# Kernel tuning notes

Hardware: AMD Instinct MI355X
Metric: run time of the kernel (lower is better)

Reference implementation:

```python
import jax, jax.numpy as jnp
import numpy as np

EMB = 300      # node embedding dim (GNNGraph default)
NL = 5         # num GNN layers
G = 4096       # number of graphs in batch
ATOM_F, ATOM_V = 9, 128   # OGB-style atom encoder: 9 categorical feats
BOND_F, BOND_V = 3, 8     # OGB-style bond encoder: 3 categorical feats
BN_EPS = 1e-5


def _bn(x, g, b, m, v):
    # BatchNorm1d in eval mode (running stats)
    return (x - m) * jax.lax.rsqrt(v + BN_EPS) * g + b


def _gnn(x, edge_index, edge_attr, batch,
         atom_emb, bond_emb, vn_emb,
         gin_eps, gin_W1, gin_b1, gin_bn1_g, gin_bn1_b, gin_bn1_m, gin_bn1_v,
         gin_W2, gin_b2, bn_g, bn_b, bn_m, bn_v,
         vn_W1, vn_b1, vn_bn1_g, vn_bn1_b, vn_bn1_m, vn_bn1_v,
         vn_W2, vn_b2, vn_bn2_g, vn_bn2_b, vn_bn2_m, vn_bn2_v):
    N = x.shape[0]
    # AtomEncoder / BondEncoder: sum of per-feature embedding lookups
    h = atom_emb[jnp.arange(ATOM_F)[None, :], x].sum(axis=1)          # [N, EMB]
    e = bond_emb[jnp.arange(BOND_F)[None, :], edge_attr].sum(axis=1)  # [E, EMB]
    row, col = edge_index[0], edge_index[1]
    # virtual node embedding, one per graph
    vn = jnp.broadcast_to(vn_emb[0], (G, EMB))
    for l in range(NL):
        h = h + vn[batch]                                   # broadcast virtual node
        # GINConv: message = relu(x_j + edge_emb), aggr = scatter-add at target
        msg = jax.nn.relu(h[row] + e)                       # [E, EMB]
        agg = jax.ops.segment_sum(msg, col, num_segments=N) # [N, EMB]
        t = (1.0 + gin_eps[l]) * h + agg
        t = jnp.dot(t, gin_W1[l]) + gin_b1[l]               # [N, 2*EMB]
        t = jax.nn.relu(_bn(t, gin_bn1_g[l], gin_bn1_b[l], gin_bn1_m[l], gin_bn1_v[l]))
        t = jnp.dot(t, gin_W2[l]) + gin_b2[l]               # [N, EMB]
        hn = _bn(t, bn_g[l], bn_b[l], bn_m[l], bn_v[l])     # outer BatchNorm
        if l < NL - 1:
            hn = jax.nn.relu(hn)                            # (dropout inactive in eval)
            # virtual node update: global_add_pool(h_list[layer]) + vn -> MLP
            pooled = jax.ops.segment_sum(h, batch, num_segments=G) + vn
            u = jnp.dot(pooled, vn_W1[l]) + vn_b1[l]
            u = jax.nn.relu(_bn(u, vn_bn1_g[l], vn_bn1_b[l], vn_bn1_m[l], vn_bn1_v[l]))
            u = jnp.dot(u, vn_W2[l]) + vn_b2[l]
            vn = jax.nn.relu(_bn(u, vn_bn2_g[l], vn_bn2_b[l], vn_bn2_m[l], vn_bn2_v[l]))
        h = hn
    # global_mean_pool over graphs
    counts = jax.ops.segment_sum(jnp.ones((N,), h.dtype), batch, num_segments=G)
    return jax.ops.segment_sum(h, batch, num_segments=G) / jnp.maximum(counts, 1.0)[:, None]


def setup_inputs() -> dict:
    key = jax.random.key(0)
    ks = iter(jax.random.split(key, 64))
    N, E = 100000, 250000
    d = {}
    d['x'] = jax.random.randint(next(ks), (N, ATOM_F), 0, ATOM_V, dtype=jnp.int32)
    d['edge_index'] = jax.random.randint(next(ks), (2, E), 0, N, dtype=jnp.int32)
    d['edge_attr'] = jax.random.randint(next(ks), (E, BOND_F), 0, BOND_V, dtype=jnp.int32)
    d['batch'] = jnp.sort(jax.random.randint(next(ks), (N,), 0, G, dtype=jnp.int32))
    s = 0.05
    d['atom_emb'] = jax.random.normal(next(ks), (ATOM_F, ATOM_V, EMB), jnp.float32) * s
    d['bond_emb'] = jax.random.normal(next(ks), (BOND_F, BOND_V, EMB), jnp.float32) * s
    d['vn_emb'] = jax.random.normal(next(ks), (1, EMB), jnp.float32) * s
    d['gin_eps'] = jax.random.normal(next(ks), (NL,), jnp.float32) * 0.01
    d['gin_W1'] = jax.random.normal(next(ks), (NL, EMB, 2 * EMB), jnp.float32) * s
    d['gin_b1'] = jax.random.normal(next(ks), (NL, 2 * EMB), jnp.float32) * s
    d['gin_bn1_g'] = 1.0 + jax.random.normal(next(ks), (NL, 2 * EMB), jnp.float32) * s
    d['gin_bn1_b'] = jax.random.normal(next(ks), (NL, 2 * EMB), jnp.float32) * s
    d['gin_bn1_m'] = jax.random.normal(next(ks), (NL, 2 * EMB), jnp.float32) * s
    d['gin_bn1_v'] = jax.random.uniform(next(ks), (NL, 2 * EMB), jnp.float32) + 0.5
    d['gin_W2'] = jax.random.normal(next(ks), (NL, 2 * EMB, EMB), jnp.float32) * s
    d['gin_b2'] = jax.random.normal(next(ks), (NL, EMB), jnp.float32) * s
    d['bn_g'] = 1.0 + jax.random.normal(next(ks), (NL, EMB), jnp.float32) * s
    d['bn_b'] = jax.random.normal(next(ks), (NL, EMB), jnp.float32) * s
    d['bn_m'] = jax.random.normal(next(ks), (NL, EMB), jnp.float32) * s
    d['bn_v'] = jax.random.uniform(next(ks), (NL, EMB), jnp.float32) + 0.5
    V = NL - 1
    d['vn_W1'] = jax.random.normal(next(ks), (V, EMB, 2 * EMB), jnp.float32) * s
    d['vn_b1'] = jax.random.normal(next(ks), (V, 2 * EMB), jnp.float32) * s
    d['vn_bn1_g'] = 1.0 + jax.random.normal(next(ks), (V, 2 * EMB), jnp.float32) * s
    d['vn_bn1_b'] = jax.random.normal(next(ks), (V, 2 * EMB), jnp.float32) * s
    d['vn_bn1_m'] = jax.random.normal(next(ks), (V, 2 * EMB), jnp.float32) * s
    d['vn_bn1_v'] = jax.random.uniform(next(ks), (V, 2 * EMB), jnp.float32) + 0.5
    d['vn_W2'] = jax.random.normal(next(ks), (V, 2 * EMB, EMB), jnp.float32) * s
    d['vn_b2'] = jax.random.normal(next(ks), (V, EMB), jnp.float32) * s
    d['vn_bn2_g'] = 1.0 + jax.random.normal(next(ks), (V, EMB), jnp.float32) * s
    d['vn_bn2_b'] = jax.random.normal(next(ks), (V, EMB), jnp.float32) * s
    d['vn_bn2_m'] = jax.random.normal(next(ks), (V, EMB), jnp.float32) * s
    d['vn_bn2_v'] = jax.random.uniform(next(ks), (V, EMB), jnp.float32) + 0.5
    return d


def reference(x, edge_index, edge_attr, batch,
              atom_emb, bond_emb, vn_emb,
              gin_eps, gin_W1, gin_b1, gin_bn1_g, gin_bn1_b, gin_bn1_m, gin_bn1_v,
              gin_W2, gin_b2, bn_g, bn_b, bn_m, bn_v,
              vn_W1, vn_b1, vn_bn1_g, vn_bn1_b, vn_bn1_m, vn_bn1_v,
              vn_W2, vn_b2, vn_bn2_g, vn_bn2_b, vn_bn2_m, vn_bn2_v):
    return _gnn(x, edge_index, edge_attr, batch,
                atom_emb, bond_emb, vn_emb,
                gin_eps, gin_W1, gin_b1, gin_bn1_g, gin_bn1_b, gin_bn1_m, gin_bn1_v,
                gin_W2, gin_b2, bn_g, bn_b, bn_m, bn_v,
                vn_W1, vn_b1, vn_bn1_g, vn_bn1_b, vn_bn1_m, vn_bn1_v,
                vn_W2, vn_b2, vn_bn2_g, vn_bn2_b, vn_bn2_m, vn_bn2_v)
```

## Files before the change

kernel.cpp:

```cpp
#include <hip/hip_runtime.h>
#include <hip/hip_bf16.h>

#define EMBD 300
#define GG   4096
#define NLAY 5
#define KP1  320
#define KP2  640
#define KT2  608
#define NP1  640
#define NP2  384
#define WPER (NP1*KP1 + NP2*KP2)

typedef unsigned short ushort_t;
typedef short short8 __attribute__((ext_vector_type(8)));
typedef short short4v __attribute__((ext_vector_type(4)));
typedef float f32x4 __attribute__((ext_vector_type(4)));

static inline int cdiv(int a, int b) { return (a + b - 1) / b; }


__device__ inline void dma16(const ushort_t* g, ushort_t* l) {
    __builtin_amdgcn_global_load_lds(
        (const __attribute__((address_space(1))) unsigned int*)g,
        (__attribute__((address_space(3))) unsigned int*)l, 16, 0, 0);
}

__device__ inline ushort_t bf16_of(float v) {
    union { __hip_bfloat16 b; ushort_t u; } c;
    c.b = __float2bfloat16(v);
    return c.u;
}

__device__ inline float bf2f(ushort_t u) {
    union { unsigned int i; float f; } c;
    c.i = ((unsigned int)u) << 16;
    return c.f;
}


__global__ void atom_encode_bf(const int* __restrict__ x, const float* __restrict__ aemb,
                               ushort_t* __restrict__ h, int N) {
    int i = blockIdx.x * blockDim.x + threadIdx.x;
    int total = N * 75;
    if (i >= total) return;
    int n = i / 75, d4 = i - n * 75;
    const int* xr = x + n * 9;
    float4 s = make_float4(0.f, 0.f, 0.f, 0.f);
    const float4* a4 = (const float4*)aemb;
#pragma unroll
    for (int f = 0; f < 9; ++f) {
        float4 v = a4[(size_t)((f << 7) + xr[f]) * 75 + d4];
        s.x += v.x; s.y += v.y; s.z += v.z; s.w += v.w;
    }
    short4v o;
    o[0] = (short)bf16_of(s.x); o[1] = (short)bf16_of(s.y);
    o[2] = (short)bf16_of(s.z); o[3] = (short)bf16_of(s.w);
    *(short4v*)(h + (size_t)n * KP1 + d4 * 4) = o;
}

__global__ void init_vn4(const float* __restrict__ vn_emb, float* __restrict__ vn) {
    int i = blockIdx.x * blockDim.x + threadIdx.x;
    if (i >= GG * 75) return;
    ((float4*)vn)[i] = ((const float4*)vn_emb)[i % 75];
}

__global__ void find_starts(const int* __restrict__ batch, int* __restrict__ starts, int N) {
    int g = blockIdx.x * blockDim.x + threadIdx.x;
    if (g > GG) return;
    int lo = 0, hi = N;
    while (lo < hi) {
        int mid = (lo + hi) >> 1;
        if (batch[mid] < g) lo = mid + 1; else hi = mid;
    }
    starts[g] = lo;
}

__global__ void bond_combo(const float* __restrict__ bemb, float* __restrict__ ebsum) {
    int i = blockIdx.x * blockDim.x + threadIdx.x;
    if (i >= 512 * EMBD) return;
    int c = i / EMBD, d = i - c * EMBD;
    int a0 = c >> 6, a1 = (c >> 3) & 7, a2 = c & 7;
    ebsum[i] = bemb[a0 * EMBD + d] + bemb[(8 + a1) * EMBD + d] + bemb[(16 + a2) * EMBD + d];
}

__global__ void conv_all(const float* __restrict__ gW1, const float* __restrict__ gW2,
                         const float* __restrict__ vW1, const float* __restrict__ vW2,
                         ushort_t* __restrict__ wh) {
    int i = blockIdx.x * blockDim.x + threadIdx.x;
    int total = WPER * 9;
    if (i >= total) return;
    int mlp = i / WPER, r = i - mlp * WPER;
    const float *W1, *W2;
    if (mlp < NLAY) {
        W1 = gW1 + (size_t)mlp * EMBD * 2 * EMBD;
        W2 = gW2 + (size_t)mlp * 2 * EMBD * EMBD;
    } else {
        int l = mlp - NLAY;
        W1 = vW1 + (size_t)l * EMBD * 2 * EMBD;
        W2 = vW2 + (size_t)l * 2 * EMBD * EMBD;
    }
    float v;
    if (r < NP1 * KP1) {
        int n = r / KP1, k = r - n * KP1;
        v = (n < 2 * EMBD && k < EMBD) ? W1[(size_t)k * (2 * EMBD) + n] : 0.f;
    } else {
        int r2 = r - NP1 * KP1;
        int n = r2 / KP2, k = r2 - n * KP2;
        v = (n < EMBD && k < 2 * EMBD) ? W2[(size_t)k * EMBD + n] : 0.f;
    }
    wh[i] = bf16_of(v);
}


__global__ void ecount(const int* __restrict__ ei, int* __restrict__ cnt, int E) {
    int e = blockIdx.x * blockDim.x + threadIdx.x;
    if (e >= E) return;
    atomicAdd(&cnt[ei[E + e]], 1);
}

__global__ void scan_part(const int* __restrict__ cnt, int* __restrict__ bsum, int N) {
    __shared__ int sh[256];
    int b = blockIdx.x, t = threadIdx.x;
    int base = b * 1024;
    int s = 0;
    for (int j = t; j < 1024; j += 256) {
        int idx = base + j;
        if (idx < N) s += cnt[idx];
    }
    sh[t] = s;
    __syncthreads();
    for (int d = 128; d > 0; d >>= 1) {
        if (t < d) sh[t] += sh[t + d];
        __syncthreads();
    }
    if (t == 0) bsum[b] = sh[0];
}

__global__ void scan_top(int* __restrict__ bsum, int nb) {
    __shared__ int sh[1024];
    int t = threadIdx.x;
    int v = (t < nb) ? bsum[t] : 0;
    sh[t] = v;
    __syncthreads();
    for (int d = 1; d < 1024; d <<= 1) {
        int u = (t >= d) ? sh[t - d] : 0;
        __syncthreads();
        sh[t] += u;
        __syncthreads();
    }
    if (t < nb) bsum[t] = sh[t] - v;
}

__global__ void scan_final(int* __restrict__ cnt, const int* __restrict__ bsum,
                           int* __restrict__ estart, int* __restrict__ cursor, int N, int E) {
    __shared__ int sh[256];
    int b = blockIdx.x, t = threadIdx.x;
    int base = b * 1024 + t * 4;
    int c[4];
    int s = 0;
#pragma unroll
    for (int j = 0; j < 4; ++j) {
        int idx = base + j;
        c[j] = (idx < N) ? cnt[idx] : 0;
        s += c[j];
    }
    sh[t] = s;
    __syncthreads();
    for (int d = 1; d < 256; d <<= 1) {
        int u = (t >= d) ? sh[t - d] : 0;
        __syncthreads();
        sh[t] += u;
        __syncthreads();
    }
    int run = sh[t] - s + bsum[b];
#pragma unroll
    for (int j = 0; j < 4; ++j) {
        int idx = base + j;
        if (idx < N) { estart[idx] = run; cursor[idx] = run; run += c[j]; }
    }
    if (b == 0 && t == 0) estart[N] = E;
}

__global__ void escatter(const int* __restrict__ ei, const int* __restrict__ ea,
                         int* __restrict__ cursor, int* __restrict__ epack, int E) {
    int e = blockIdx.x * blockDim.x + threadIdx.x;
    if (e >= E) return;
    int c = ei[E + e];
    int p = atomicAdd(&cursor[c], 1);
    epack[p] = (ei[e] << 9) | (ea[3 * e] << 6) | (ea[3 * e + 1] << 3) | ea[3 * e + 2];
}


__global__ void pool_prep(ushort_t* __restrict__ h, const float* __restrict__ vn,
                          const int* __restrict__ starts, ushort_t* __restrict__ vnaB) {
    int g = blockIdx.x * 4 + threadIdx.x / 80;
    int slot = threadIdx.x % 80;
    if (g >= GG || slot >= 75) return;
    float4 vng = ((const float4*)vn)[(size_t)g * 75 + slot];
    int s0 = starts[g], s1 = starts[g + 1];
    float4 s = make_float4(0.f, 0.f, 0.f, 0.f);
    for (int n = s0; n < s1; ++n) {
        short4v* hp = (short4v*)(h + (size_t)n * KP1 + slot * 4);
        short4v hv = *hp;
        float v0 = bf2f((ushort_t)hv[0]) + vng.x;
        float v1 = bf2f((ushort_t)hv[1]) + vng.y;
        float v2 = bf2f((ushort_t)hv[2]) + vng.z;
        float v3 = bf2f((ushort_t)hv[3]) + vng.w;
        short4v o;
        o[0] = (short)bf16_of(v0); o[1] = (short)bf16_of(v1);
        o[2] = (short)bf16_of(v2); o[3] = (short)bf16_of(v3);
        *hp = o;
        s.x += v0; s.y += v1; s.z += v2; s.w += v3;
    }
    short4v o;
    o[0] = (short)bf16_of(s.x + vng.x); o[1] = (short)bf16_of(s.y + vng.y);
    o[2] = (short)bf16_of(s.z + vng.z); o[3] = (short)bf16_of(s.w + vng.w);
    *(short4v*)(vnaB + (size_t)g * KP1 + slot * 4) = o;
}

__global__ void prep_vn(ushort_t* __restrict__ h, const float* __restrict__ vn,
                        const int* __restrict__ batch, int N) {
    int i = blockIdx.x * blockDim.x + threadIdx.x;
    int total = N * 75;
    if (i >= total) return;
    int n = i / 75, d4 = i - n * 75;
    float4 vv = ((const float4*)vn)[(size_t)batch[n] * 75 + d4];
    short4v hv = *(short4v*)(h + (size_t)n * KP1 + d4 * 4);
    short4v o;
    o[0] = (short)bf16_of(bf2f((ushort_t)hv[0]) + vv.x);
    o[1] = (short)bf16_of(bf2f((ushort_t)hv[1]) + vv.y);
    o[2] = (short)bf16_of(bf2f((ushort_t)hv[2]) + vv.z);
    o[3] = (short)bf16_of(bf2f((ushort_t)hv[3]) + vv.w);
    *(short4v*)(h + (size_t)n * KP1 + d4 * 4) = o;
}

__global__ void pool_mean(const ushort_t* __restrict__ h, const int* __restrict__ starts,
                          float* __restrict__ out) {
    int g = blockIdx.x * 4 + threadIdx.x / 80;
    int slot = threadIdx.x % 80;
    if (g >= GG || slot >= 75) return;
    int s0 = starts[g], s1 = starts[g + 1];
    float4 s = make_float4(0.f, 0.f, 0.f, 0.f);
    for (int n = s0; n < s1; ++n) {
        short4v hv = *(const short4v*)(h + (size_t)n * KP1 + slot * 4);
        s.x += bf2f((ushort_t)hv[0]);
        s.y += bf2f((ushort_t)hv[1]);
        s.z += bf2f((ushort_t)hv[2]);
        s.w += bf2f((ushort_t)hv[3]);
    }
    float inv = 1.0f / fmaxf((float)(s1 - s0), 1.0f);
    float4 o = make_float4(s.x * inv, s.y * inv, s.z * inv, s.w * inv);
    ((float4*)out)[(size_t)g * 75 + slot] = o;
}

#define NPB 4

__global__ void aggregate(const ushort_t* __restrict__ h, const float* __restrict__ ebsum,
                          const int* __restrict__ estart, const int* __restrict__ epack,
                          const float* __restrict__ epsp,
                          ushort_t* __restrict__ aggB, int N) {
    int n = blockIdx.x * NPB + threadIdx.x / 80;
    int slot = threadIdx.x % 80;
    if (n >= N) return;
    float4 acc = make_float4(0.f, 0.f, 0.f, 0.f);
    if (slot < 75) {
        const float4* b4 = (const float4*)ebsum;
        float ce = 1.0f + *epsp;
        short4v hv = *(const short4v*)(h + (size_t)n * KP1 + slot * 4);
        acc.x = ce * bf2f((ushort_t)hv[0]);
        acc.y = ce * bf2f((ushort_t)hv[1]);
        acc.z = ce * bf2f((ushort_t)hv[2]);
        acc.w = ce * bf2f((ushort_t)hv[3]);
        int p0 = estart[n], p1 = estart[n + 1];
        int p = p0;
        for (; p + 2 <= p1; p += 2) {
            int e0 = epack[p], e1 = epack[p + 1];
            short4v xv0 = *(const short4v*)(h + (size_t)(e0 >> 9) * KP1 + slot * 4);
            short4v xv1 = *(const short4v*)(h + (size_t)(e1 >> 9) * KP1 + slot * 4);
            float4 ev0 = b4[(size_t)(e0 & 511) * 75 + slot];
            float4 ev1 = b4[(size_t)(e1 & 511) * 75 + slot];
            acc.x += fmaxf(bf2f((ushort_t)xv0[0]) + ev0.x, 0.f) + fmaxf(bf2f((ushort_t)xv1[0]) + ev1.x, 0.f);
            acc.y += fmaxf(bf2f((ushort_t)xv0[1]) + ev0.y, 0.f) + fmaxf(bf2f((ushort_t)xv1[1]) + ev1.y, 0.f);
            acc.z += fmaxf(bf2f((ushort_t)xv0[2]) + ev0.z, 0.f) + fmaxf(bf2f((ushort_t)xv1[2]) + ev1.z, 0.f);
            acc.w += fmaxf(bf2f((ushort_t)xv0[3]) + ev0.w, 0.f) + fmaxf(bf2f((ushort_t)xv1[3]) + ev1.w, 0.f);
        }
        if (p < p1) {
            int e0 = epack[p];
            short4v xv0 = *(const short4v*)(h + (size_t)(e0 >> 9) * KP1 + slot * 4);
            float4 ev0 = b4[(size_t)(e0 & 511) * 75 + slot];
            acc.x += fmaxf(bf2f((ushort_t)xv0[0]) + ev0.x, 0.f);
            acc.y += fmaxf(bf2f((ushort_t)xv0[1]) + ev0.y, 0.f);
            acc.z += fmaxf(bf2f((ushort_t)xv0[2]) + ev0.z, 0.f);
            acc.w += fmaxf(bf2f((ushort_t)xv0[3]) + ev0.w, 0.f);
        }
    }
    short4v bv4;
    bv4[0] = (short)bf16_of(acc.x);
    bv4[1] = (short)bf16_of(acc.y);
    bv4[2] = (short)bf16_of(acc.z);
    bv4[3] = (short)bf16_of(acc.w);
    *(short4v*)(aggB + (size_t)n * KP1 + slot * 4) = bv4;
}

#define BMg 128
#define BNg 128
#define STG (BMg * 32)

__global__ __launch_bounds__(256) void gemm_as(
    const ushort_t* __restrict__ A, int KPA,
    const ushort_t* __restrict__ B, int KPB,
    const float* __restrict__ bias, const float* __restrict__ gg,
    const float* __restrict__ bb, const float* __restrict__ bm,
    const float* __restrict__ bv,
    int Mc, int NnReal, int relu, int nb, int mb,
    float* __restrict__ outF, int ldF,
    ushort_t* __restrict__ outB, int ldP)
{
    __shared__ ushort_t smem[4 * STG];

    int id = blockIdx.x;
    int hi = id / (8 * nb);
    int rem = id - hi * 8 * nb;
    int xcd = rem & 7;
    int nblk = rem >> 3;
    int mblk = hi * 8 + xcd;
    if (mblk >= mb) return;

    const int tid = threadIdx.x;
    const int lane = tid & 63;
    const int w = tid >> 6;
    const int m0 = mblk * BMg;
    const int n0 = nblk * BNg;
    const int wm = (w & 1) * 64;
    const int wn = (w >> 1) * 64;

    const ushort_t* gA[2];
    const ushort_t* gB[2];
    int lbase[2];
#pragma unroll
    for (int i = 0; i < 2; ++i) {
        int s = tid + 256 * i;
        int m = s >> 2, qp = s & 3;
        int q = (qp - (m >> 1)) & 3;
        int msrc = (m0 + m < Mc) ? (m0 + m) : (Mc - 1);
        gA[i] = A + (size_t)msrc * KPA + 8 * q;
        gB[i] = B + (size_t)(n0 + m) * KPB + 8 * q;
        lbase[i] = (w * 64 + 256 * i) * 8;
    }

    f32x4 acc[4][4];
#pragma unroll
    for (int a = 0; a < 4; ++a)
#pragma unroll
        for (int b = 0; b < 4; ++b) acc[a][b] = (f32x4)(0.f);

    const int q = lane >> 4;
    const int c16 = lane & 15;
    const int kt = KPA >> 5;

#pragma unroll
    for (int i = 0; i < 2; ++i) {
        dma16(gA[i], smem + lbase[i]);           gA[i] += 32;
        dma16(gB[i], smem + 2 * STG + lbase[i]); gB[i] += 32;
    }
    __syncthreads();

    for (int t = 0; t < kt; ++t) {
        int cur = t & 1, nxt = cur ^ 1;
        if (t + 1 < kt) {
#pragma unroll
            for (int i = 0; i < 2; ++i) {
                dma16(gA[i], smem + nxt * STG + lbase[i]);       gA[i] += 32;
                dma16(gB[i], smem + (2 + nxt) * STG + lbase[i]); gB[i] += 32;
            }
        }
        const ushort_t* sAc = smem + cur * STG;
        const ushort_t* sBc = smem + (2 + cur) * STG;
        short8 av[4], bhv[4];
#pragma unroll
        for (int tt = 0; tt < 4; ++tt) {
            int m = wm + tt * 16 + c16;
            int q2 = (q + (m >> 1)) & 3;
            av[tt] = *(const short8*)(sAc + m * 32 + q2 * 8);
        }
#pragma unroll
        for (int uu = 0; uu < 4; ++uu) {
            int n = wn + uu * 16 + c16;
            int q2 = (q + (n >> 1)) & 3;
            bhv[uu] = *(const short8*)(sBc + n * 32 + q2 * 8);
        }
#pragma unroll
        for (int tt = 0; tt < 4; ++tt)
#pragma unroll
            for (int uu = 0; uu < 4; ++uu)
                acc[tt][uu] = __builtin_amdgcn_mfma_f32_16x16x32_bf16(av[tt], bhv[uu], acc[tt][uu], 0, 0, 0);
        __syncthreads();
    }

    float sc[4], sh[4];
#pragma unroll
    for (int uu = 0; uu < 4; ++uu) {
        int gn = n0 + wn + uu * 16 + c16;
        if (gn < NnReal) {
            float s = gg[gn] * rsqrtf(bv[gn] + 1e-5f);
            sc[uu] = s;
            sh[uu] = bb[gn] + (bias[gn] - bm[gn]) * sc[uu];
        } else { sc[uu] = 0.f; sh[uu] = 0.f; }
    }

    if (outB) {
        const int rot = q * 16;
#pragma unroll
        for (int uu = 0; uu < 4; ++uu) {
#pragma unroll
            for (int tt = 0; tt < 4; ++tt) {
                int row = wm + tt * 16 + q * 4;
#pragma unroll
                for (int r = 0; r < 4; ++r) {
                    float y = acc[tt][uu][r] * sc[uu] + sh[uu];
                    if (relu) y = fmaxf(y, 0.f);
                    int col_s = (wn + uu * 16 + c16 + rot) & 127;
                    smem[(row + r) * 128 + col_s] = bf16_of(y);
                }
            }
        }
        __syncthreads();
#pragma unroll
        for (int j = 0; j < 8; ++j) {
            int row = j * 16 + q * 4 + w;
            int gm = m0 + row;
            int gcl = c16 * 8;
            if (gm < Mc && n0 + gcl + 8 <= ldP) {
                short8 v = *(const short8*)(smem + row * 128 + ((gcl + rot) & 127));
                *(short8*)(outB + (size_t)gm * ldP + n0 + gcl) = v;
            }
        }
    } else {
#pragma unroll
        for (int uu = 0; uu < 4; ++uu) {
            int gn = n0 + wn + uu * 16 + c16;
#pragma unroll
            for (int tt = 0; tt < 4; ++tt) {
                int rbase = m0 + wm + tt * 16 + q * 4;
#pragma unroll
                for (int r = 0; r < 4; ++r) {
                    int gm = rbase + r;
                    if (gm >= Mc) continue;
                    float y = acc[tt][uu][r] * sc[uu] + sh[uu];
                    if (relu) y = fmaxf(y, 0.f);
                    if (gn < NnReal) outF[(size_t)gm * ldF + gn] = y;
                }
            }
        }
    }
}


struct MlpP {
    const float *b1, *g1, *be1, *m1, *v1;
    const float *b2, *g2, *be2, *m2, *v2;
};

static void run_mlp(hipStream_t stream, const ushort_t* inB, int M,
                    const ushort_t* wh, int mlp,
                    ushort_t* tB, int CH,
                    const MlpP& W, ushort_t* outB, int relu2) {
    const ushort_t* w1 = wh + (size_t)mlp * WPER;
    const ushort_t* w2 = w1 + NP1 * KP1;
    for (int c0 = 0; c0 < M; c0 += CH) {
        int Mc = (M - c0 < CH) ? (M - c0) : CH;
        int mb = cdiv(Mc, BMg);
        int mbp = cdiv(mb, 8) * 8;
        {
            int nb = NP1 / BNg;
            gemm_as<<<nb * mbp, 256, 0, stream>>>(
                inB + (size_t)c0 * KP1, KP1, w1, KP1,
                W.b1, W.g1, W.be1, W.m1, W.v1,
                Mc, 2 * EMBD, 1, nb, mb,
                nullptr, 0, tB, KT2);
        }
        {
            int nb = NP2 / BNg;
            gemm_as<<<nb * mbp, 256, 0, stream>>>(
                tB, KT2, w2, KP2,
                W.b2, W.g2, W.be2, W.m2, W.v2,
                Mc, EMBD, relu2, nb, mb,
                nullptr, 0, outB + (size_t)c0 * KP1, KP1);
        }
    }
}


extern "C" void kernel_launch(void* const* d_in, const int* in_sizes, int n_in,
                              void* d_out, int out_size, void* d_ws, size_t ws_size,
                              hipStream_t stream) {
    const int*   x        = (const int*)d_in[0];
    const int*   ei       = (const int*)d_in[1];
    const int*   ea       = (const int*)d_in[2];
    const int*   batch    = (const int*)d_in[3];
    const float* atom_emb = (const float*)d_in[4];
    const float* bond_emb = (const float*)d_in[5];
    const float* vn_emb   = (const float*)d_in[6];
    const float* gin_eps  = (const float*)d_in[7];
    const float* gin_W1   = (const float*)d_in[8];
    const float* gin_b1   = (const float*)d_in[9];
    const float* gin_bn1g = (const float*)d_in[10];
    const float* gin_bn1b = (const float*)d_in[11];
    const float* gin_bn1m = (const float*)d_in[12];
    const float* gin_bn1v = (const float*)d_in[13];
    const float* gin_W2   = (const float*)d_in[14];
    const float* gin_b2   = (const float*)d_in[15];
    const float* bn_g     = (const float*)d_in[16];
    const float* bn_b     = (const float*)d_in[17];
    const float* bn_m     = (const float*)d_in[18];
    const float* bn_v     = (const float*)d_in[19];
    const float* vn_W1    = (const float*)d_in[20];
    const float* vn_b1    = (const float*)d_in[21];
    const float* vn_bn1g  = (const float*)d_in[22];
    const float* vn_bn1b  = (const float*)d_in[23];
    const float* vn_bn1m  = (const float*)d_in[24];
    const float* vn_bn1v  = (const float*)d_in[25];
    const float* vn_W2    = (const float*)d_in[26];
    const float* vn_b2    = (const float*)d_in[27];
    const float* vn_bn2g  = (const float*)d_in[28];
    const float* vn_bn2b  = (const float*)d_in[29];
    const float* vn_bn2m  = (const float*)d_in[30];
    const float* vn_bn2v  = (const float*)d_in[31];

    const int N = in_sizes[3];
    const int E = in_sizes[1] / 2;
    const int NB = cdiv(N, 1024);

    char* base = (char*)d_ws;
    size_t off = 0;
    ushort_t* hbuf = (ushort_t*)(base + off); off += (size_t)N * KP1 * 2;
    ushort_t* aggB = (ushort_t*)(base + off); off += (size_t)N * KP1 * 2;
    float* vnbuf   = (float*)(base + off);    off += (size_t)GG * EMBD * 4;
    int*   starts  = (int*)(base + off);      off += 4104 * 4;
    int*   cnt     = (int*)(base + off);      off += (size_t)N * 4;
    int*   estart  = (int*)(base + off);      off += ((size_t)N + 8) * 4;
    int*   bsum    = (int*)(base + off);      off += 1032 * 4;
    int*   epack   = (int*)(base + off);      off += (size_t)E * 4;
    float* ebsum   = (float*)(base + off);    off += (size_t)512 * EMBD * 4;
    ushort_t* whA  = (ushort_t*)(base + off); off += (size_t)9 * WPER * 2;
    ushort_t* vnaB = (ushort_t*)(base + off); off += (size_t)GG * KP1 * 2;
    off = (off + 255) & ~(size_t)255;

    size_t avail = (ws_size > off) ? ws_size - off : 0;
    int CH = (int)(avail / (KT2 * 2));
    CH &= ~255;
    if (CH >= N) CH = (N + 255) & ~255;
    else if (CH >= (N + 1) / 2) CH = (((N + 1) / 2) + 255) & ~255;
    if (CH < 2048) CH = 2048;
    ushort_t* tB = (ushort_t*)(base + off);

    const int BLK = 256;
    int ne4 = N * 75;

    find_starts<<<cdiv(GG + 1, BLK), BLK, 0, stream>>>(batch, starts, N);
    atom_encode_bf<<<cdiv(ne4, BLK), BLK, 0, stream>>>(x, atom_emb, hbuf, N);
    init_vn4<<<cdiv(GG * 75, BLK), BLK, 0, stream>>>(vn_emb, vnbuf);
    bond_combo<<<cdiv(512 * EMBD, BLK), BLK, 0, stream>>>(bond_emb, ebsum);
    conv_all<<<cdiv(9 * WPER, BLK), BLK, 0, stream>>>(gin_W1, gin_W2, vn_W1, vn_W2, whA);
    (void)hipMemsetAsync(cnt, 0, (size_t)N * 4, stream);
    (void)hipMemsetAsync(vnaB, 0, (size_t)GG * KP1 * 2, stream);
    ecount<<<cdiv(E, BLK), BLK, 0, stream>>>(ei, cnt, E);
    scan_part<<<NB, 256, 0, stream>>>(cnt, bsum, N);
    scan_top<<<1, 1024, 0, stream>>>(bsum, NB);
    scan_final<<<NB, 256, 0, stream>>>(cnt, bsum, estart, cnt , N, E);
    escatter<<<cdiv(E, BLK), BLK, 0, stream>>>(ei, ea, cnt , epack, E);

    for (int l = 0; l < NLAY; ++l) {
        int last = (l == NLAY - 1);

        if (!last)
            pool_prep<<<GG / 4, 320, 0, stream>>>(hbuf, vnbuf, starts, vnaB);
        else
            prep_vn<<<cdiv(ne4, BLK), BLK, 0, stream>>>(hbuf, vnbuf, batch, N);

        aggregate<<<cdiv(N, NPB), NPB * 80, 0, stream>>>(
            hbuf, ebsum, estart, epack, gin_eps + l, aggB, N);

        MlpP Wn = { gin_b1 + (size_t)l * 2 * EMBD,
                    gin_bn1g + (size_t)l * 2 * EMBD, gin_bn1b + (size_t)l * 2 * EMBD,
                    gin_bn1m + (size_t)l * 2 * EMBD, gin_bn1v + (size_t)l * 2 * EMBD,
                    gin_b2 + (size_t)l * EMBD,
                    bn_g + (size_t)l * EMBD, bn_b + (size_t)l * EMBD,
                    bn_m + (size_t)l * EMBD, bn_v + (size_t)l * EMBD };
        run_mlp(stream, aggB, N, whA, l, tB, CH, Wn, hbuf, last ? 0 : 1);

        if (!last) {
            const ushort_t* w1 = whA + (size_t)(NLAY + l) * WPER;
            const ushort_t* w2 = w1 + NP1 * KP1;
            int mb = cdiv(GG, BMg), mbp = cdiv(mb, 8) * 8;
            gemm_as<<<(NP1 / BNg) * mbp, 256, 0, stream>>>(
                vnaB, KP1, w1, KP1,
                vn_b1 + (size_t)l * 2 * EMBD, vn_bn1g + (size_t)l * 2 * EMBD,
                vn_bn1b + (size_t)l * 2 * EMBD, vn_bn1m + (size_t)l * 2 * EMBD,
                vn_bn1v + (size_t)l * 2 * EMBD,
                GG, 2 * EMBD, 1, NP1 / BNg, mb,
                nullptr, 0, tB, KT2);
            gemm_as<<<(NP2 / BNg) * mbp, 256, 0, stream>>>(
                tB, KT2, w2, KP2,
                vn_b2 + (size_t)l * EMBD, vn_bn2g + (size_t)l * EMBD,
                vn_bn2b + (size_t)l * EMBD, vn_bn2m + (size_t)l * EMBD,
                vn_bn2v + (size_t)l * EMBD,
                GG, EMBD, 1, NP2 / BNg, mb,
                vnbuf, EMBD, nullptr, 0);
        }
    }

    pool_mean<<<GG / 4, 320, 0, stream>>>(hbuf, starts, (float*)d_out);
}
```

Baseline: 1.565 ms.

## Fuse virtual-node broadcast into MLP GEMM epilogue and drop h rewrite passes

```diff
diff --git a/kernel.cpp b/kernel.cpp
--- a/kernel.cpp
+++ b/kernel.cpp
@@ -39,13 +39,14 @@
 
 
 __global__ void atom_encode_bf(const int* __restrict__ x, const float* __restrict__ aemb,
+                               const float* __restrict__ vn_emb,
                                ushort_t* __restrict__ h, int N) {
     int i = blockIdx.x * blockDim.x + threadIdx.x;
     int total = N * 75;
     if (i >= total) return;
     int n = i / 75, d4 = i - n * 75;
     const int* xr = x + n * 9;
-    float4 s = make_float4(0.f, 0.f, 0.f, 0.f);
+    float4 s = ((const float4*)vn_emb)[d4];
     const float4* a4 = (const float4*)aemb;
 #pragma unroll
     for (int f = 0; f < 9; ++f) {
@@ -191,7 +192,7 @@
 }
 
 
-__global__ void pool_prep(ushort_t* __restrict__ h, const float* __restrict__ vn,
+__global__ void pool_only(const ushort_t* __restrict__ h, const float* __restrict__ vn,
                           const int* __restrict__ starts, ushort_t* __restrict__ vnaB) {
     int g = blockIdx.x * 4 + threadIdx.x / 80;
     int slot = threadIdx.x % 80;
@@ -200,38 +201,16 @@
     int s0 = starts[g], s1 = starts[g + 1];
     float4 s = make_float4(0.f, 0.f, 0.f, 0.f);
     for (int n = s0; n < s1; ++n) {
-        short4v* hp = (short4v*)(h + (size_t)n * KP1 + slot * 4);
-        short4v hv = *hp;
-        float v0 = bf2f((ushort_t)hv[0]) + vng.x;
-        float v1 = bf2f((ushort_t)hv[1]) + vng.y;
-        float v2 = bf2f((ushort_t)hv[2]) + vng.z;
-        float v3 = bf2f((ushort_t)hv[3]) + vng.w;
-        short4v o;
-        o[0] = (short)bf16_of(v0); o[1] = (short)bf16_of(v1);
-        o[2] = (short)bf16_of(v2); o[3] = (short)bf16_of(v3);
-        *hp = o;
-        s.x += v0; s.y += v1; s.z += v2; s.w += v3;
+        short4v hv = *(const short4v*)(h + (size_t)n * KP1 + slot * 4);
+        s.x += bf2f((ushort_t)hv[0]);
+        s.y += bf2f((ushort_t)hv[1]);
+        s.z += bf2f((ushort_t)hv[2]);
+        s.w += bf2f((ushort_t)hv[3]);
     }
     short4v o;
     o[0] = (short)bf16_of(s.x + vng.x); o[1] = (short)bf16_of(s.y + vng.y);
     o[2] = (short)bf16_of(s.z + vng.z); o[3] = (short)bf16_of(s.w + vng.w);
     *(short4v*)(vnaB + (size_t)g * KP1 + slot * 4) = o;
-}
-
-__global__ void prep_vn(ushort_t* __restrict__ h, const float* __restrict__ vn,
-                        const int* __restrict__ batch, int N) {
-    int i = blockIdx.x * blockDim.x + threadIdx.x;
-    int total = N * 75;
-    if (i >= total) return;
-    int n = i / 75, d4 = i - n * 75;
-    float4 vv = ((const float4*)vn)[(size_t)batch[n] * 75 + d4];
-    short4v hv = *(short4v*)(h + (size_t)n * KP1 + d4 * 4);
-    short4v o;
-    o[0] = (short)bf16_of(bf2f((ushort_t)hv[0]) + vv.x);
-    o[1] = (short)bf16_of(bf2f((ushort_t)hv[1]) + vv.y);
-    o[2] = (short)bf16_of(bf2f((ushort_t)hv[2]) + vv.z);
-    o[3] = (short)bf16_of(bf2f((ushort_t)hv[3]) + vv.w);
-    *(short4v*)(h + (size_t)n * KP1 + d4 * 4) = o;
 }
 
 __global__ void pool_mean(const ushort_t* __restrict__ h, const int* __restrict__ starts,
@@ -313,6 +292,7 @@
     const float* __restrict__ bb, const float* __restrict__ bm,
     const float* __restrict__ bv,
     int Mc, int NnReal, int relu, int nb, int mb,
+    const float* __restrict__ vnadd, const int* __restrict__ batchp,
     float* __restrict__ outF, int ldF,
     ushort_t* __restrict__ outB, int ldP)
 {
@@ -432,6 +412,27 @@
             int gcl = c16 * 8;
             if (gm < Mc && n0 + gcl + 8 <= ldP) {
                 short8 v = *(const short8*)(smem + row * 128 + ((gcl + rot) & 127));
+                if (vnadd) {
+                    const float* vrow = vnadd + (size_t)batchp[gm] * EMBD;
+                    int colb = n0 + gcl;
+                    if (colb + 8 <= EMBD) {
+                        float4 a = *(const float4*)(vrow + colb);
+                        float4 b = *(const float4*)(vrow + colb + 4);
+                        v[0] = (short)bf16_of(bf2f((ushort_t)v[0]) + a.x);
+                        v[1] = (short)bf16_of(bf2f((ushort_t)v[1]) + a.y);
+                        v[2] = (short)bf16_of(bf2f((ushort_t)v[2]) + a.z);
+                        v[3] = (short)bf16_of(bf2f((ushort_t)v[3]) + a.w);
+                        v[4] = (short)bf16_of(bf2f((ushort_t)v[4]) + b.x);
+                        v[5] = (short)bf16_of(bf2f((ushort_t)v[5]) + b.y);
+                        v[6] = (short)bf16_of(bf2f((ushort_t)v[6]) + b.z);
+                        v[7] = (short)bf16_of(bf2f((ushort_t)v[7]) + b.w);
+                    } else if (colb < EMBD) {
+#pragma unroll
+                        for (int k = 0; k < 8; ++k)
+                            if (colb + k < EMBD)
+                                v[k] = (short)bf16_of(bf2f((ushort_t)v[k]) + vrow[colb + k]);
+                    }
+                }
                 *(short8*)(outB + (size_t)gm * ldP + n0 + gcl) = v;
             }
         }
@@ -464,7 +465,8 @@
 static void run_mlp(hipStream_t stream, const ushort_t* inB, int M,
                     const ushort_t* wh, int mlp,
                     ushort_t* tB, int CH,
-                    const MlpP& W, ushort_t* outB, int relu2) {
+                    const MlpP& W, ushort_t* outB, int relu2,
+                    const float* vnadd, const int* batch) {
     const ushort_t* w1 = wh + (size_t)mlp * WPER;
     const ushort_t* w2 = w1 + NP1 * KP1;
     for (int c0 = 0; c0 < M; c0 += CH) {
@@ -477,6 +479,7 @@
                 inB + (size_t)c0 * KP1, KP1, w1, KP1,
                 W.b1, W.g1, W.be1, W.m1, W.v1,
                 Mc, 2 * EMBD, 1, nb, mb,
+                nullptr, nullptr,
                 nullptr, 0, tB, KT2);
         }
         {
@@ -485,6 +488,7 @@
                 tB, KT2, w2, KP2,
                 W.b2, W.g2, W.be2, W.m2, W.v2,
                 Mc, EMBD, relu2, nb, mb,
+                vnadd, vnadd ? (batch + c0) : nullptr,
                 nullptr, 0, outB + (size_t)c0 * KP1, KP1);
         }
     }
@@ -558,7 +562,7 @@
     int ne4 = N * 75;
 
     find_starts<<<cdiv(GG + 1, BLK), BLK, 0, stream>>>(batch, starts, N);
-    atom_encode_bf<<<cdiv(ne4, BLK), BLK, 0, stream>>>(x, atom_emb, hbuf, N);
+    atom_encode_bf<<<cdiv(ne4, BLK), BLK, 0, stream>>>(x, atom_emb, vn_emb, hbuf, N);
     init_vn4<<<cdiv(GG * 75, BLK), BLK, 0, stream>>>(vn_emb, vnbuf);
     bond_combo<<<cdiv(512 * EMBD, BLK), BLK, 0, stream>>>(bond_emb, ebsum);
     conv_all<<<cdiv(9 * WPER, BLK), BLK, 0, stream>>>(gin_W1, gin_W2, vn_W1, vn_W2, whA);
@@ -573,23 +577,8 @@
     for (int l = 0; l < NLAY; ++l) {
         int last = (l == NLAY - 1);
 
-        if (!last)
-            pool_prep<<<GG / 4, 320, 0, stream>>>(hbuf, vnbuf, starts, vnaB);
-        else
-            prep_vn<<<cdiv(ne4, BLK), BLK, 0, stream>>>(hbuf, vnbuf, batch, N);
-
-        aggregate<<<cdiv(N, NPB), NPB * 80, 0, stream>>>(
-            hbuf, ebsum, estart, epack, gin_eps + l, aggB, N);
-
-        MlpP Wn = { gin_b1 + (size_t)l * 2 * EMBD,
-                    gin_bn1g + (size_t)l * 2 * EMBD, gin_bn1b + (size_t)l * 2 * EMBD,
-                    gin_bn1m + (size_t)l * 2 * EMBD, gin_bn1v + (size_t)l * 2 * EMBD,
-                    gin_b2 + (size_t)l * EMBD,
-                    bn_g + (size_t)l * EMBD, bn_b + (size_t)l * EMBD,
-                    bn_m + (size_t)l * EMBD, bn_v + (size_t)l * EMBD };
-        run_mlp(stream, aggB, N, whA, l, tB, CH, Wn, hbuf, last ? 0 : 1);
-
         if (!last) {
+            pool_only<<<GG / 4, 320, 0, stream>>>(hbuf, vnbuf, starts, vnaB);
             const ushort_t* w1 = whA + (size_t)(NLAY + l) * WPER;
             const ushort_t* w2 = w1 + NP1 * KP1;
             int mb = cdiv(GG, BMg), mbp = cdiv(mb, 8) * 8;
@@ -599,6 +588,7 @@
                 vn_bn1b + (size_t)l * 2 * EMBD, vn_bn1m + (size_t)l * 2 * EMBD,
                 vn_bn1v + (size_t)l * 2 * EMBD,
                 GG, 2 * EMBD, 1, NP1 / BNg, mb,
+                nullptr, nullptr,
                 nullptr, 0, tB, KT2);
             gemm_as<<<(NP2 / BNg) * mbp, 256, 0, stream>>>(
                 tB, KT2, w2, KP2,
@@ -606,8 +596,21 @@
                 vn_bn2b + (size_t)l * EMBD, vn_bn2m + (size_t)l * EMBD,
                 vn_bn2v + (size_t)l * EMBD,
                 GG, EMBD, 1, NP2 / BNg, mb,
+                nullptr, nullptr,
                 vnbuf, EMBD, nullptr, 0);
         }
+
+        aggregate<<<cdiv(N, NPB), NPB * 80, 0, stream>>>(
+            hbuf, ebsum, estart, epack, gin_eps + l, aggB, N);
+
+        MlpP Wn = { gin_b1 + (size_t)l * 2 * EMBD,
+                    gin_bn1g + (size_t)l * 2 * EMBD, gin_bn1b + (size_t)l * 2 * EMBD,
+                    gin_bn1m + (size_t)l * 2 * EMBD, gin_bn1v + (size_t)l * 2 * EMBD,
+                    gin_b2 + (size_t)l * EMBD,
+                    bn_g + (size_t)l * EMBD, bn_b + (size_t)l * EMBD,
+                    bn_m + (size_t)l * EMBD, bn_v + (size_t)l * EMBD };
+        run_mlp(stream, aggB, N, whA, l, tB, CH, Wn, hbuf, last ? 0 : 1,
+                last ? nullptr : vnbuf, batch);
     }
 
     pool_mean<<<GG / 4, 320, 0, stream>>>(hbuf, starts, (float*)d_out);
```

After: 1.563 ms. No clear change (-0.2%).
